# Kernel optimization log

Hardware: AMD Instinct MI355X
Metric: run time of the kernel (lower is better)

## Reference

```python
import jax, jax.numpy as jnp
import numpy as np

N_P, N_A, D_MP = 200000, 100000, 64   # paper nodes, author nodes, metapath embed dim
E = 1200000                            # nnz per adjacency op
F_P, F_A = 256, 128                    # raw feature dims


def _spmm(row, col, val, z, n_out):
    # Sparse [n_out, n_in] @ dense [n_in, d]: out[i] = sum_{e: row[e]==i} val[e] * z[col[e]]
    return jax.ops.segment_sum(val[:, None] * z[col], row, num_segments=n_out)


def setup_inputs() -> dict:
    key = jax.random.key(0)
    k = jax.random.split(key, 10)
    return {
        "x_paper": jax.random.normal(k[0], (N_P, F_P), jnp.float32),
        "x_author": jax.random.normal(k[1], (N_A, F_A), jnp.float32),
        "W_paper": jax.random.normal(k[2], (F_P, D_MP), jnp.float32) / np.float32(np.sqrt(F_P)),
        "W_author": jax.random.normal(k[3], (F_A, D_MP), jnp.float32) / np.float32(np.sqrt(F_A)),
        "pa_row": jax.random.randint(k[4], (E,), 0, N_A, jnp.int32),
        "pa_col": jax.random.randint(k[5], (E,), 0, N_P, jnp.int32),
        "pa_val": jax.random.uniform(k[6], (E,), jnp.float32),
        "ap_row": jax.random.randint(k[7], (E,), 0, N_P, jnp.int32),
        "ap_col": jax.random.randint(k[8], (E,), 0, N_A, jnp.int32),
        "ap_val": jax.random.uniform(k[9], (E,), jnp.float32),
    }


def reference(x_paper, x_author, W_paper, W_author,
              pa_row, pa_col, pa_val, ap_row, ap_col, ap_val):
    # per-node-type projection (nn.Linear, no bias)
    zp = x_paper @ W_paper    # [N_P, D_MP]
    za = x_author @ W_author  # [N_A, D_MP]

    # metapath P-A-P: ops = [pa (N_A x N_P), ap (N_P x N_A)]
    h = _spmm(pa_row, pa_col, pa_val, zp, N_A)
    pap = _spmm(ap_row, ap_col, ap_val, h, N_P)

    # metapath P-A-P-A-P: 4 chained SpMMs
    h2 = _spmm(pa_row, pa_col, pa_val, pap, N_A)
    papap = _spmm(ap_row, ap_col, ap_val, h2, N_P)

    # metapath A-P-A: ops = [ap (N_P x N_A), pa (N_A x N_P)]
    g = _spmm(ap_row, ap_col, ap_val, za, N_P)
    apa = _spmm(pa_row, pa_col, pa_val, g, N_A)

    return (pap, papap, apa)
```

## Files before the change

kernel.cpp:

```cpp
#include <hip/hip_runtime.h>
#include <hip/hip_fp16.h>

#define NP 200000
#define NA 100000
#define NE 1200000


__global__ __launch_bounds__(256) void hist_k(const int* __restrict__ row, int* __restrict__ cnt, int n) {
    int i = blockIdx.x * blockDim.x + threadIdx.x;
    int stride = gridDim.x * blockDim.x;
    for (; i < n; i += stride) atomicAdd(&cnt[row[i]], 1);
}

__global__ __launch_bounds__(256) void scan1_k(const int* __restrict__ in, int* __restrict__ out,
                                               int* __restrict__ bsums, int n) {
    __shared__ int lds[256];
    int t = threadIdx.x;
    int base = blockIdx.x * 1024 + t * 4;
    int v0 = (base + 0 < n) ? in[base + 0] : 0;
    int v1 = (base + 1 < n) ? in[base + 1] : 0;
    int v2 = (base + 2 < n) ? in[base + 2] : 0;
    int v3 = (base + 3 < n) ? in[base + 3] : 0;
    lds[t] = v0 + v1 + v2 + v3;
    __syncthreads();
    for (int off = 1; off < 256; off <<= 1) {
        int x = (t >= off) ? lds[t - off] : 0;
        __syncthreads();
        lds[t] += x;
        __syncthreads();
    }
    if (t == 255) bsums[blockIdx.x] = lds[255];
    int run = (t == 0) ? 0 : lds[t - 1];
    if (base + 0 < n) out[base + 0] = run; run += v0;
    if (base + 1 < n) out[base + 1] = run; run += v1;
    if (base + 2 < n) out[base + 2] = run; run += v2;
    if (base + 3 < n) out[base + 3] = run;
}

__global__ void scan2_k(int* bsums, int nb) {
    __shared__ int lds[256];
    int t = threadIdx.x;
    int v = (t < nb) ? bsums[t] : 0;
    lds[t] = v;
    __syncthreads();
    for (int off = 1; off < 256; off <<= 1) {
        int x = (t >= off) ? lds[t - off] : 0;
        __syncthreads();
        lds[t] += x;
        __syncthreads();
    }
    if (t < nb) bsums[t] = (t == 0) ? 0 : lds[t - 1];
}

__global__ __launch_bounds__(256) void scan3_k(int* __restrict__ out, const int* __restrict__ bsums, int n) {
    int add = bsums[blockIdx.x];
    int base = blockIdx.x * 1024 + threadIdx.x * 4;
#pragma unroll
    for (int j = 0; j < 4; j++)
        if (base + j < n) out[base + j] += add;
}

__global__ __launch_bounds__(256) void scatter_k(const int* __restrict__ row, const int* __restrict__ col,
                                                 const float* __restrict__ val, const int* __restrict__ off,
                                                 int* __restrict__ cursor, int2* __restrict__ csr, int n) {
    int i = blockIdx.x * blockDim.x + threadIdx.x;
    int stride = gridDim.x * blockDim.x;
    for (; i < n; i += stride) {
        int r = row[i];
        int pos = off[r] + atomicAdd(&cursor[r], 1);
        csr[pos] = make_int2(col[i], __float_as_int(val[i]));
    }
}


__device__ __forceinline__ void fma_h8(float acc[8], float v, uint4 r) {
    __half2 h0 = *(__half2*)&r.x;
    __half2 h1 = *(__half2*)&r.y;
    __half2 h2 = *(__half2*)&r.z;
    __half2 h3 = *(__half2*)&r.w;
    float2 f0 = __half22float2(h0);
    float2 f1 = __half22float2(h1);
    float2 f2 = __half22float2(h2);
    float2 f3 = __half22float2(h3);
    acc[0] = fmaf(v, f0.x, acc[0]);
    acc[1] = fmaf(v, f0.y, acc[1]);
    acc[2] = fmaf(v, f1.x, acc[2]);
    acc[3] = fmaf(v, f1.y, acc[3]);
    acc[4] = fmaf(v, f2.x, acc[4]);
    acc[5] = fmaf(v, f2.y, acc[5]);
    acc[6] = fmaf(v, f3.x, acc[6]);
    acc[7] = fmaf(v, f3.y, acc[7]);
}

__device__ __forceinline__ void store_h8(uint4* out16, int g, int l, const float acc[8]) {
    __half2 p0 = __floats2half2_rn(acc[0], acc[1]);
    __half2 p1 = __floats2half2_rn(acc[2], acc[3]);
    __half2 p2 = __floats2half2_rn(acc[4], acc[5]);
    __half2 p3 = __floats2half2_rn(acc[6], acc[7]);
    uint4 o;
    o.x = *(unsigned*)&p0;
    o.y = *(unsigned*)&p1;
    o.z = *(unsigned*)&p2;
    o.w = *(unsigned*)&p3;
    out16[(size_t)g * 8 + l] = o;
}

__device__ __forceinline__ void store_f8(float4* out32, int g, int l, const float acc[8]) {
    out32[(size_t)g * 16 + l * 2 + 0] = make_float4(acc[0], acc[1], acc[2], acc[3]);
    out32[(size_t)g * 16 + l * 2 + 1] = make_float4(acc[4], acc[5], acc[6], acc[7]);
}

__global__ __launch_bounds__(256) void spmm_k(const int2* __restrict__ csr, const int* __restrict__ off,
                                              const int* __restrict__ cnt, const uint4* __restrict__ z,
                                              float4* __restrict__ out32, uint4* __restrict__ out16,
                                              int nrows) {
    int g = blockIdx.x * 32 + (threadIdx.x >> 3);
    int l = threadIdx.x & 7;
    if (g >= nrows) return;
    int start = off[g], deg = cnt[g];
    float acc[8];
#pragma unroll
    for (int i = 0; i < 8; i++) acc[i] = 0.f;

    if (deg > 0) {
        int2 e[8];
#pragma unroll
        for (int k = 0; k < 8; k++) e[k] = csr[start + min(k, deg - 1)];
        for (int j = 0; j < deg; j += 8) {
            uint4 r[8];
#pragma unroll
            for (int k = 0; k < 8; k++) r[k] = z[e[k].x * 8 + l];
            float v[8];
#pragma unroll
            for (int k = 0; k < 8; k++) v[k] = (j + k < deg) ? __int_as_float(e[k].y) : 0.f;
            int2 en[8];
            bool more = (j + 8) < deg;
            if (more) {
#pragma unroll
                for (int k = 0; k < 8; k++) en[k] = csr[start + min(j + 8 + k, deg - 1)];
            }
#pragma unroll
            for (int k = 0; k < 8; k++) fma_h8(acc, v[k], r[k]);
            if (more) {
#pragma unroll
                for (int k = 0; k < 8; k++) e[k] = en[k];
            }
        }
    }
    if (out32) store_f8(out32, g, l, acc);
    if (out16) store_h8(out16, g, l, acc);
}

__global__ __launch_bounds__(256) void spmm2_k(const int2* __restrict__ csr, const int* __restrict__ off,
                                               const int* __restrict__ cnt,
                                               const uint4* __restrict__ zA, const uint4* __restrict__ zB,
                                               float4* __restrict__ outA32, uint4* __restrict__ outA16,
                                               float4* __restrict__ outB32, uint4* __restrict__ outB16,
                                               int nrows) {
    int g = blockIdx.x * 32 + (threadIdx.x >> 3);
    int l = threadIdx.x & 7;
    if (g >= nrows) return;
    int start = off[g], deg = cnt[g];
    float accA[8], accB[8];
#pragma unroll
    for (int i = 0; i < 8; i++) { accA[i] = 0.f; accB[i] = 0.f; }

    if (deg > 0) {
        int2 e[8];
#pragma unroll
        for (int k = 0; k < 8; k++) e[k] = csr[start + min(k, deg - 1)];
        for (int j = 0; j < deg; j += 8) {
            uint4 rA[8], rB[8];
#pragma unroll
            for (int k = 0; k < 8; k++) {
                int idx = e[k].x * 8 + l;
                rA[k] = zA[idx];
                rB[k] = zB[idx];
            }
            float v[8];
#pragma unroll
            for (int k = 0; k < 8; k++) v[k] = (j + k < deg) ? __int_as_float(e[k].y) : 0.f;
            int2 en[8];
            bool more = (j + 8) < deg;
            if (more) {
#pragma unroll
                for (int k = 0; k < 8; k++) en[k] = csr[start + min(j + 8 + k, deg - 1)];
            }
#pragma unroll
            for (int k = 0; k < 8; k++) {
                fma_h8(accA, v[k], rA[k]);
                fma_h8(accB, v[k], rB[k]);
            }
            if (more) {
#pragma unroll
                for (int k = 0; k < 8; k++) e[k] = en[k];
            }
        }
    }
    if (outA32) store_f8(outA32, g, l, accA);
    if (outA16) store_h8(outA16, g, l, accA);
    if (outB32) store_f8(outB32, g, l, accB);
    if (outB16) store_h8(outB16, g, l, accB);
}


template <int K>
__global__ __launch_bounds__(256) void gemm64_k(const float* __restrict__ x, const float* __restrict__ w,
                                                __half* __restrict__ z16, int nrows) {
    __shared__ float xs[32][256];
    __shared__ float wsh[32][64];
    int t = threadIdx.x;
    int tx = t & 7;
    int ty = t >> 3;
    int r0 = blockIdx.x * 256;

    float acc[8][8];
#pragma unroll
    for (int i = 0; i < 8; i++)
#pragma unroll
        for (int j = 0; j < 8; j++) acc[i][j] = 0.f;

    for (int k0 = 0; k0 < K; k0 += 32) {
        __syncthreads();
        {
            int row = r0 + t;
            float4 f[8];
            if (row < nrows) {
                const float* xp = x + (size_t)row * K + k0;
#pragma unroll
                for (int q = 0; q < 8; q++) f[q] = *(const float4*)&xp[q * 4];
            } else {
#pragma unroll
                for (int q = 0; q < 8; q++) f[q] = make_float4(0.f, 0.f, 0.f, 0.f);
            }
#pragma unroll
            for (int q = 0; q < 8; q++) {
                xs[q * 4 + 0][t] = f[q].x;
                xs[q * 4 + 1][t] = f[q].y;
                xs[q * 4 + 2][t] = f[q].z;
                xs[q * 4 + 3][t] = f[q].w;
            }
            const float* wp = w + (size_t)k0 * 64;
            float* wflat = &wsh[0][0];
            *(float4*)&wflat[t * 8 + 0] = *(const float4*)&wp[t * 8 + 0];
            *(float4*)&wflat[t * 8 + 4] = *(const float4*)&wp[t * 8 + 4];
        }
        __syncthreads();
#pragma unroll 8
        for (int kk = 0; kk < 32; kk++) {
            float a[8], b[8];
            *(float4*)&a[0] = *(float4*)&xs[kk][ty * 8 + 0];
            *(float4*)&a[4] = *(float4*)&xs[kk][ty * 8 + 4];
            *(float4*)&b[0] = *(float4*)&wsh[kk][tx * 8 + 0];
            *(float4*)&b[4] = *(float4*)&wsh[kk][tx * 8 + 4];
#pragma unroll
            for (int i = 0; i < 8; i++)
#pragma unroll
                for (int j = 0; j < 8; j++) acc[i][j] = fmaf(a[i], b[j], acc[i][j]);
        }
    }

    int row0 = r0 + ty * 8;
    if (row0 < nrows) {
#pragma unroll
        for (int i = 0; i < 8; i++) {
            __half2 p0 = __floats2half2_rn(acc[i][0], acc[i][1]);
            __half2 p1 = __floats2half2_rn(acc[i][2], acc[i][3]);
            __half2 p2 = __floats2half2_rn(acc[i][4], acc[i][5]);
            __half2 p3 = __floats2half2_rn(acc[i][6], acc[i][7]);
            uint4 o;
            o.x = *(unsigned*)&p0;
            o.y = *(unsigned*)&p1;
            o.z = *(unsigned*)&p2;
            o.w = *(unsigned*)&p3;
            *(uint4*)&z16[(size_t)(row0 + i) * 64 + tx * 8] = o;
        }
    }
}


extern "C" void kernel_launch(void* const* d_in, const int* in_sizes, int n_in,
                              void* d_out, int out_size, void* d_ws, size_t ws_size,
                              hipStream_t stream) {
    const float* x_paper  = (const float*)d_in[0];
    const float* x_author = (const float*)d_in[1];
    const float* W_paper  = (const float*)d_in[2];
    const float* W_author = (const float*)d_in[3];
    const int*   pa_row   = (const int*)d_in[4];
    const int*   pa_col   = (const int*)d_in[5];
    const float* pa_val   = (const float*)d_in[6];
    const int*   ap_row   = (const int*)d_in[7];
    const int*   ap_col   = (const int*)d_in[8];
    const float* ap_val   = (const float*)d_in[9];

    char* ws = (char*)d_ws;
    size_t o = 0;
    auto alloc = [&](size_t bytes) -> char* {
        char* p = ws + o;
        o += (bytes + 255) & ~(size_t)255;
        return p;
    };
    __half* zp16  = (__half*)alloc((size_t)NP * 64 * 2);
    __half* za16  = (__half*)alloc((size_t)NA * 64 * 2);
    __half* h16   = (__half*)alloc((size_t)NA * 64 * 2);
    __half* pap16 = (__half*)alloc((size_t)NP * 64 * 2);
    int2*  csr_pa = (int2*)alloc((size_t)NE * 8);
    int2*  csr_ap = (int2*)alloc((size_t)NE * 8);
    int* cnt_pa = (int*)alloc(NA * 4);
    int* off_pa = (int*)alloc(NA * 4);
    int* cnt_ap = (int*)alloc(NP * 4);
    int* off_ap = (int*)alloc(NP * 4);
    int* cursor = (int*)alloc(NP * 4);
    int* bsums  = (int*)alloc(1024 * 4);

    float* out_pap   = (float*)d_out;
    float* out_papap = out_pap + (size_t)NP * 64;
    float* out_apa   = out_papap + (size_t)NP * 64;

    const int nb_a = (NA + 1023) / 1024;
    const int nb_p = (NP + 1023) / 1024;

    hipMemsetAsync(cnt_pa, 0, NA * 4, stream);
    hipMemsetAsync(cnt_ap, 0, NP * 4, stream);
    hist_k<<<1024, 256, 0, stream>>>(pa_row, cnt_pa, NE);
    hist_k<<<1024, 256, 0, stream>>>(ap_row, cnt_ap, NE);

    scan1_k<<<nb_a, 256, 0, stream>>>(cnt_pa, off_pa, bsums, NA);
    scan2_k<<<1, 256, 0, stream>>>(bsums, nb_a);
    scan3_k<<<nb_a, 256, 0, stream>>>(off_pa, bsums, NA);
    hipMemsetAsync(cursor, 0, NA * 4, stream);
    scatter_k<<<1024, 256, 0, stream>>>(pa_row, pa_col, pa_val, off_pa, cursor, csr_pa, NE);

    scan1_k<<<nb_p, 256, 0, stream>>>(cnt_ap, off_ap, bsums, NP);
    scan2_k<<<1, 256, 0, stream>>>(bsums, nb_p);
    scan3_k<<<nb_p, 256, 0, stream>>>(off_ap, bsums, NP);
    hipMemsetAsync(cursor, 0, NP * 4, stream);
    scatter_k<<<1024, 256, 0, stream>>>(ap_row, ap_col, ap_val, off_ap, cursor, csr_ap, NE);

    gemm64_k<256><<<(NP + 255) / 256, 256, 0, stream>>>(x_paper, W_paper, zp16, NP);
    gemm64_k<128><<<(NA + 255) / 256, 256, 0, stream>>>(x_author, W_author, za16, NA);

    spmm_k<<<NA / 32, 256, 0, stream>>>(csr_pa, off_pa, cnt_pa, (const uint4*)zp16,
                                        nullptr, (uint4*)h16, NA);
    spmm2_k<<<NP / 32, 256, 0, stream>>>(csr_ap, off_ap, cnt_ap,
                                         (const uint4*)h16, (const uint4*)za16,
                                         (float4*)out_pap, (uint4*)pap16,
                                         nullptr, (uint4*)zp16, NP);
    spmm2_k<<<NA / 32, 256, 0, stream>>>(csr_pa, off_pa, cnt_pa,
                                         (const uint4*)pap16, (const uint4*)zp16,
                                         nullptr, (uint4*)h16,
                                         (float4*)out_apa, nullptr, NA);
    spmm_k<<<NP / 32, 256, 0, stream>>>(csr_ap, off_ap, cnt_ap, (const uint4*)h16,
                                        (float4*)out_papap, nullptr, NP);
}
```

Before: 844.6 us.

## Merge CSR build for both adjacencies and switch projection GEMM to MFMA

The two COO-to-CSR conversions (histogram, scan, scatter) are merged into single launches over a concatenated row space, with scan2 widened to 512 threads. The FP32 LDS-tiled projection GEMMs are replaced by one fused launch using fp16 MFMA 16x16x32 intrinsics, with a small kernel that transposes and converts the weights to fp16. This aims to cut launch count and move the dense projection onto matrix cores, at the cost of rounding x to fp16 before the multiply and using uncoalesced scalar half stores for the output.

```diff
diff --git a/kernel.cpp b/kernel.cpp
--- a/kernel.cpp
+++ b/kernel.cpp
@@ -4,12 +4,22 @@
 #define NP 200000
 #define NA 100000
 #define NE 1200000
-
-
-__global__ __launch_bounds__(256) void hist_k(const int* __restrict__ row, int* __restrict__ cnt, int n) {
+#define NTOT (NA + NP)
+#define NBP_GEMM 3125
+#define NBA_GEMM 1563
+
+typedef _Float16 half8 __attribute__((ext_vector_type(8)));
+typedef float f32x4 __attribute__((ext_vector_type(4)));
+
+
+__global__ __launch_bounds__(256) void hist2_k(const int* __restrict__ pa_row, const int* __restrict__ ap_row,
+                                               int* __restrict__ cnt_all) {
     int i = blockIdx.x * blockDim.x + threadIdx.x;
     int stride = gridDim.x * blockDim.x;
-    for (; i < n; i += stride) atomicAdd(&cnt[row[i]], 1);
+    for (; i < 2 * NE; i += stride) {
+        if (i < NE) atomicAdd(&cnt_all[pa_row[i]], 1);
+        else        atomicAdd(&cnt_all[NA + ap_row[i - NE]], 1);
+    }
 }
 
 __global__ __launch_bounds__(256) void scan1_k(const int* __restrict__ in, int* __restrict__ out,
@@ -38,18 +48,18 @@
 }
 
 __global__ void scan2_k(int* bsums, int nb) {
-    __shared__ int lds[256];
+    __shared__ int lds[512];
     int t = threadIdx.x;
     int v = (t < nb) ? bsums[t] : 0;
     lds[t] = v;
     __syncthreads();
-    for (int off = 1; off < 256; off <<= 1) {
+    for (int off = 1; off < 512; off <<= 1) {
         int x = (t >= off) ? lds[t - off] : 0;
         __syncthreads();
         lds[t] += x;
         __syncthreads();
     }
-    if (t < nb) bsums[t] = (t == 0) ? 0 : lds[t - 1];
+    if (t < nb) bsums[t] = lds[t] - v;
 }
 
 __global__ __launch_bounds__(256) void scan3_k(int* __restrict__ out, const int* __restrict__ bsums, int n) {
@@ -60,15 +70,24 @@
         if (base + j < n) out[base + j] += add;
 }
 
-__global__ __launch_bounds__(256) void scatter_k(const int* __restrict__ row, const int* __restrict__ col,
-                                                 const float* __restrict__ val, const int* __restrict__ off,
-                                                 int* __restrict__ cursor, int2* __restrict__ csr, int n) {
+__global__ __launch_bounds__(256) void scatter2_k(const int* __restrict__ pa_row, const int* __restrict__ pa_col,
+                                                  const float* __restrict__ pa_val,
+                                                  const int* __restrict__ ap_row, const int* __restrict__ ap_col,
+                                                  const float* __restrict__ ap_val,
+                                                  const int* __restrict__ off_all, int* __restrict__ cursor,
+                                                  int2* __restrict__ csr_all) {
     int i = blockIdx.x * blockDim.x + threadIdx.x;
     int stride = gridDim.x * blockDim.x;
-    for (; i < n; i += stride) {
-        int r = row[i];
-        int pos = off[r] + atomicAdd(&cursor[r], 1);
-        csr[pos] = make_int2(col[i], __float_as_int(val[i]));
+    for (; i < 2 * NE; i += stride) {
+        if (i < NE) {
+            int r = pa_row[i];
+            int pos = off_all[r] + atomicAdd(&cursor[r], 1);
+            csr_all[pos] = make_int2(pa_col[i], __float_as_int(pa_val[i]));
+        } else {
+            int r = NA + ap_row[i - NE];
+            int pos = off_all[r] + atomicAdd(&cursor[r], 1);
+            csr_all[pos] = make_int2(ap_col[i - NE], __float_as_int(ap_val[i - NE]));
+        }
     }
 }
 
@@ -204,76 +223,77 @@
 }
 
 
-template <int K>
-__global__ __launch_bounds__(256) void gemm64_k(const float* __restrict__ x, const float* __restrict__ w,
-                                                __half* __restrict__ z16, int nrows) {
-    __shared__ float xs[32][256];
-    __shared__ float wsh[32][64];
-    int t = threadIdx.x;
-    int tx = t & 7;
-    int ty = t >> 3;
-    int r0 = blockIdx.x * 256;
-
-    float acc[8][8];
-#pragma unroll
-    for (int i = 0; i < 8; i++)
-#pragma unroll
-        for (int j = 0; j < 8; j++) acc[i][j] = 0.f;
+__global__ __launch_bounds__(256) void wconv_k(const float* __restrict__ Wp, const float* __restrict__ Wa,
+                                               __half* __restrict__ wtP, __half* __restrict__ wtA) {
+    int i = blockIdx.x * 256 + threadIdx.x;
+    int stride = gridDim.x * 256;
+    for (int idx = i; idx < 64 * 256; idx += stride) {
+        int c = idx >> 8, k = idx & 255;
+        wtP[idx] = (__half)Wp[k * 64 + c];
+    }
+    for (int idx = i; idx < 64 * 128; idx += stride) {
+        int c = idx >> 7, k = idx & 127;
+        wtA[idx] = (__half)Wa[k * 64 + c];
+    }
+}
+
+__global__ __launch_bounds__(256) void gemm_mfma_k(const float* __restrict__ xP, const float* __restrict__ xA,
+                                                   const __half* __restrict__ wtP, const __half* __restrict__ wtA,
+                                                   __half* __restrict__ zP, __half* __restrict__ zA) {
+    int b = blockIdx.x;
+    const float* x;
+    const __half* wt;
+    __half* z;
+    int K, nrows, r0;
+    if (b < NBP_GEMM) { x = xP; wt = wtP; z = zP; K = 256; nrows = NP; r0 = b * 64; }
+    else              { x = xA; wt = wtA; z = zA; K = 128; nrows = NA; r0 = (b - NBP_GEMM) * 64; }
+
+    int w = threadIdx.x >> 6;
+    int l = threadIdx.x & 63;
+    int arow = r0 + w * 16 + (l & 15);
+    int kq = (l >> 4) * 8;
+
+    f32x4 acc0 = {0.f, 0.f, 0.f, 0.f};
+    f32x4 acc1 = {0.f, 0.f, 0.f, 0.f};
+    f32x4 acc2 = {0.f, 0.f, 0.f, 0.f};
+    f32x4 acc3 = {0.f, 0.f, 0.f, 0.f};
 
     for (int k0 = 0; k0 < K; k0 += 32) {
-        __syncthreads();
-        {
-            int row = r0 + t;
-            float4 f[8];
-            if (row < nrows) {
-                const float* xp = x + (size_t)row * K + k0;
-#pragma unroll
-                for (int q = 0; q < 8; q++) f[q] = *(const float4*)&xp[q * 4];
-            } else {
-#pragma unroll
-                for (int q = 0; q < 8; q++) f[q] = make_float4(0.f, 0.f, 0.f, 0.f);
-            }
-#pragma unroll
-            for (int q = 0; q < 8; q++) {
-                xs[q * 4 + 0][t] = f[q].x;
-                xs[q * 4 + 1][t] = f[q].y;
-                xs[q * 4 + 2][t] = f[q].z;
-                xs[q * 4 + 3][t] = f[q].w;
-            }
-            const float* wp = w + (size_t)k0 * 64;
-            float* wflat = &wsh[0][0];
-            *(float4*)&wflat[t * 8 + 0] = *(const float4*)&wp[t * 8 + 0];
-            *(float4*)&wflat[t * 8 + 4] = *(const float4*)&wp[t * 8 + 4];
-        }
-        __syncthreads();
-#pragma unroll 8
-        for (int kk = 0; kk < 32; kk++) {
-            float a[8], b[8];
-            *(float4*)&a[0] = *(float4*)&xs[kk][ty * 8 + 0];
-            *(float4*)&a[4] = *(float4*)&xs[kk][ty * 8 + 4];
-            *(float4*)&b[0] = *(float4*)&wsh[kk][tx * 8 + 0];
-            *(float4*)&b[4] = *(float4*)&wsh[kk][tx * 8 + 4];
-#pragma unroll
-            for (int i = 0; i < 8; i++)
-#pragma unroll
-                for (int j = 0; j < 8; j++) acc[i][j] = fmaf(a[i], b[j], acc[i][j]);
-        }
-    }
-
-    int row0 = r0 + ty * 8;
-    if (row0 < nrows) {
-#pragma unroll
-        for (int i = 0; i < 8; i++) {
-            __half2 p0 = __floats2half2_rn(acc[i][0], acc[i][1]);
-            __half2 p1 = __floats2half2_rn(acc[i][2], acc[i][3]);
-            __half2 p2 = __floats2half2_rn(acc[i][4], acc[i][5]);
-            __half2 p3 = __floats2half2_rn(acc[i][6], acc[i][7]);
-            uint4 o;
-            o.x = *(unsigned*)&p0;
-            o.y = *(unsigned*)&p1;
-            o.z = *(unsigned*)&p2;
-            o.w = *(unsigned*)&p3;
-            *(uint4*)&z16[(size_t)(row0 + i) * 64 + tx * 8] = o;
+        half8 a;
+        if (arow < nrows) {
+            const float* xp = x + (size_t)arow * K + k0 + kq;
+            float4 f0 = *(const float4*)xp;
+            float4 f1 = *(const float4*)(xp + 4);
+            a[0] = (_Float16)f0.x; a[1] = (_Float16)f0.y;
+            a[2] = (_Float16)f0.z; a[3] = (_Float16)f0.w;
+            a[4] = (_Float16)f1.x; a[5] = (_Float16)f1.y;
+            a[6] = (_Float16)f1.z; a[7] = (_Float16)f1.w;
+        } else {
+#pragma unroll
+            for (int j = 0; j < 8; j++) a[j] = (_Float16)0.f;
+        }
+        const __half* wbase = wt + (size_t)(l & 15) * K + k0 + kq;
+        half8 b0 = *(const half8*)(wbase);
+        half8 b1 = *(const half8*)(wbase + (size_t)16 * K);
+        half8 b2 = *(const half8*)(wbase + (size_t)32 * K);
+        half8 b3 = *(const half8*)(wbase + (size_t)48 * K);
+        acc0 = __builtin_amdgcn_mfma_f32_16x16x32_f16(a, b0, acc0, 0, 0, 0);
+        acc1 = __builtin_amdgcn_mfma_f32_16x16x32_f16(a, b1, acc1, 0, 0, 0);
+        acc2 = __builtin_amdgcn_mfma_f32_16x16x32_f16(a, b2, acc2, 0, 0, 0);
+        acc3 = __builtin_amdgcn_mfma_f32_16x16x32_f16(a, b3, acc3, 0, 0, 0);
+    }
+
+    int orow0 = r0 + w * 16 + (l >> 4) * 4;
+    int col = l & 15;
+#pragma unroll
+    for (int i = 0; i < 4; i++) {
+        int r = orow0 + i;
+        if (r < nrows) {
+            __half* zr = z + (size_t)r * 64;
+            zr[col +  0] = (__half)acc0[i];
+            zr[col + 16] = (__half)acc1[i];
+            zr[col + 32] = (__half)acc2[i];
+            zr[col + 48] = (__half)acc3[i];
         }
     }
 }
@@ -304,52 +324,47 @@
     __half* za16  = (__half*)alloc((size_t)NA * 64 * 2);
     __half* h16   = (__half*)alloc((size_t)NA * 64 * 2);
     __half* pap16 = (__half*)alloc((size_t)NP * 64 * 2);
-    int2*  csr_pa = (int2*)alloc((size_t)NE * 8);
-    int2*  csr_ap = (int2*)alloc((size_t)NE * 8);
-    int* cnt_pa = (int*)alloc(NA * 4);
-    int* off_pa = (int*)alloc(NA * 4);
-    int* cnt_ap = (int*)alloc(NP * 4);
-    int* off_ap = (int*)alloc(NP * 4);
-    int* cursor = (int*)alloc(NP * 4);
-    int* bsums  = (int*)alloc(1024 * 4);
+    int2*  csr_all = (int2*)alloc((size_t)2 * NE * 8);
+    int* cnt_all = (int*)alloc(NTOT * 4);
+    int* off_all = (int*)alloc(NTOT * 4);
+    int* cursor  = (int*)alloc(NTOT * 4);
+    int* bsums   = (int*)alloc(1024 * 4);
+    __half* wtP  = (__half*)alloc(64 * 256 * 2);
+    __half* wtA  = (__half*)alloc(64 * 128 * 2);
 
     float* out_pap   = (float*)d_out;
     float* out_papap = out_pap + (size_t)NP * 64;
     float* out_apa   = out_papap + (size_t)NP * 64;
 
-    const int nb_a = (NA + 1023) / 1024;
-    const int nb_p = (NP + 1023) / 1024;
-
-    hipMemsetAsync(cnt_pa, 0, NA * 4, stream);
-    hipMemsetAsync(cnt_ap, 0, NP * 4, stream);
-    hist_k<<<1024, 256, 0, stream>>>(pa_row, cnt_pa, NE);
-    hist_k<<<1024, 256, 0, stream>>>(ap_row, cnt_ap, NE);
-
-    scan1_k<<<nb_a, 256, 0, stream>>>(cnt_pa, off_pa, bsums, NA);
-    scan2_k<<<1, 256, 0, stream>>>(bsums, nb_a);
-    scan3_k<<<nb_a, 256, 0, stream>>>(off_pa, bsums, NA);
-    hipMemsetAsync(cursor, 0, NA * 4, stream);
-    scatter_k<<<1024, 256, 0, stream>>>(pa_row, pa_col, pa_val, off_pa, cursor, csr_pa, NE);
-
-    scan1_k<<<nb_p, 256, 0, stream>>>(cnt_ap, off_ap, bsums, NP);
-    scan2_k<<<1, 256, 0, stream>>>(bsums, nb_p);
-    scan3_k<<<nb_p, 256, 0, stream>>>(off_ap, bsums, NP);
-    hipMemsetAsync(cursor, 0, NP * 4, stream);
-    scatter_k<<<1024, 256, 0, stream>>>(ap_row, ap_col, ap_val, off_ap, cursor, csr_ap, NE);
-
-    gemm64_k<256><<<(NP + 255) / 256, 256, 0, stream>>>(x_paper, W_paper, zp16, NP);
-    gemm64_k<128><<<(NA + 255) / 256, 256, 0, stream>>>(x_author, W_author, za16, NA);
-
-    spmm_k<<<NA / 32, 256, 0, stream>>>(csr_pa, off_pa, cnt_pa, (const uint4*)zp16,
+    const int nb_tot = (NTOT + 1023) / 1024;
+
+    hipMemsetAsync(cnt_all, 0, NTOT * 4, stream);
+    hist2_k<<<1024, 256, 0, stream>>>(pa_row, ap_row, cnt_all);
+    scan1_k<<<nb_tot, 256, 0, stream>>>(cnt_all, off_all, bsums, NTOT);
+    scan2_k<<<1, 512, 0, stream>>>(bsums, nb_tot);
+    scan3_k<<<nb_tot, 256, 0, stream>>>(off_all, bsums, NTOT);
+    hipMemsetAsync(cursor, 0, NTOT * 4, stream);
+    scatter2_k<<<1024, 256, 0, stream>>>(pa_row, pa_col, pa_val, ap_row, ap_col, ap_val,
+                                         off_all, cursor, csr_all);
+
+    wconv_k<<<64, 256, 0, stream>>>(W_paper, W_author, wtP, wtA);
+    gemm_mfma_k<<<NBP_GEMM + NBA_GEMM, 256, 0, stream>>>(x_paper, x_author, wtP, wtA, zp16, za16);
+
+    const int* off_pa = off_all;
+    const int* cnt_pa = cnt_all;
+    const int* off_ap = off_all + NA;
+    const int* cnt_ap = cnt_all + NA;
+
+    spmm_k<<<NA / 32, 256, 0, stream>>>(csr_all, off_pa, cnt_pa, (const uint4*)zp16,
                                         nullptr, (uint4*)h16, NA);
-    spmm2_k<<<NP / 32, 256, 0, stream>>>(csr_ap, off_ap, cnt_ap,
+    spmm2_k<<<NP / 32, 256, 0, stream>>>(csr_all, off_ap, cnt_ap,
                                          (const uint4*)h16, (const uint4*)za16,
                                          (float4*)out_pap, (uint4*)pap16,
                                          nullptr, (uint4*)zp16, NP);
-    spmm2_k<<<NA / 32, 256, 0, stream>>>(csr_pa, off_pa, cnt_pa,
+    spmm2_k<<<NA / 32, 256, 0, stream>>>(csr_all, off_pa, cnt_pa,
                                          (const uint4*)pap16, (const uint4*)zp16,
                                          nullptr, (uint4*)h16,
                                          (float4*)out_apa, nullptr, NA);
-    spmm_k<<<NP / 32, 256, 0, stream>>>(csr_ap, off_ap, cnt_ap, (const uint4*)h16,
+    spmm_k<<<NP / 32, 256, 0, stream>>>(csr_all, off_ap, cnt_ap, (const uint4*)h16,
                                         (float4*)out_papap, nullptr, NP);
 }
```

Measured after the change: 784.3 us. -7.1%, faster.
